# Optimization experiments

Measured on AMD Instinct MI355X. Metric: run time of the kernel, lower is better.

The kernel has to match this reference:

```python
import jax, jax.numpy as jnp
import numpy as np

B, I, H = 32768, 256, 512

def setup_inputs() -> dict:
    key = jax.random.key(0)
    ks = jax.random.split(key, 12)
    s_lstm = 1.0 / np.sqrt(H)
    inp = {
        "inputs": jax.random.normal(ks[0], (B, I), dtype=jnp.float32),
        "h0": jax.random.normal(ks[1], (B, H), dtype=jnp.float32),
        "c0": jax.random.normal(ks[2], (B, H), dtype=jnp.float32),
        "ts": jax.random.uniform(ks[3], (B, 2), dtype=jnp.float32),
        # LSTMCell params (torch layout: [4H, in], gate order i,f,g,o)
        "W_ih": jax.random.uniform(ks[4], (4 * H, I), minval=-s_lstm, maxval=s_lstm, dtype=jnp.float32),
        "W_hh": jax.random.uniform(ks[5], (4 * H, H), minval=-s_lstm, maxval=s_lstm, dtype=jnp.float32),
        "b_ih": jax.random.uniform(ks[6], (4 * H,), minval=-s_lstm, maxval=s_lstm, dtype=jnp.float32),
        "b_hh": jax.random.uniform(ks[7], (4 * H,), minval=-s_lstm, maxval=s_lstm, dtype=jnp.float32),
        # ODE vector field: Linear(H,H) -> Tanh -> Linear(H,H)
        "W1": jax.random.uniform(ks[8], (H, H), minval=-s_lstm, maxval=s_lstm, dtype=jnp.float32),
        "b1": jax.random.uniform(ks[9], (H,), minval=-s_lstm, maxval=s_lstm, dtype=jnp.float32),
        "W2": jax.random.uniform(ks[10], (H, H), minval=-s_lstm, maxval=s_lstm, dtype=jnp.float32),
        "b2": jax.random.uniform(ks[11], (H,), minval=-s_lstm, maxval=s_lstm, dtype=jnp.float32),
    }
    return inp


def _lstm_cell(x, h, c, W_ih, W_hh, b_ih, b_hh):
    z = x @ W_ih.T + b_ih + h @ W_hh.T + b_hh  # [B, 4H]
    i, f, g, o = jnp.split(z, 4, axis=-1)
    i = jax.nn.sigmoid(i)
    f = jax.nn.sigmoid(f)
    g = jnp.tanh(g)
    o = jax.nn.sigmoid(o)
    c2 = f * c + i * g
    h2 = o * jnp.tanh(c2)
    return h2, c2


def reference(inputs, h0, c0, ts, W_ih, W_hh, b_ih, b_hh, W1, b1, W2, b2):
    # two sequential LSTMCell updates with the same input
    h1, c1 = _lstm_cell(inputs, h0, c0, W_ih, W_hh, b_ih, b_hh)
    new_h, new_c = _lstm_cell(inputs, h1, c1, W_ih, W_hh, b_ih, b_hh)

    # autonomous vector field f(h) = W2 tanh(W1 h + b1) + b2
    def f(h):
        return jnp.tanh(h @ W1.T + b1) @ W2.T + b2

    # batched single RK4 step from ts[:,0] to ts[:,1] (fused over batch)
    dt = (ts[:, 1] - ts[:, 0])[:, None]  # [B,1]
    k1 = f(new_h)
    k2 = f(new_h + 0.5 * dt * k1)
    k3 = f(new_h + 0.5 * dt * k2)
    k4 = f(new_h + dt * k3)
    ht = new_h + (dt / 6.0) * (k1 + 2.0 * k2 + 2.0 * k3 + k4)
    return (ht, new_c)
```

## Files before the change

### kernel.cpp

```cpp
#include <hip/hip_runtime.h>
#include <math.h>

#define BATCH 32768
#define ISZ   256
#define HSZ   512
#define KC    768

typedef __attribute__((ext_vector_type(8))) short bf16x8;
typedef __attribute__((ext_vector_type(4))) float f32x4;

static __device__ unsigned short g_xbf[(size_t)BATCH * ISZ];
static __device__ unsigned short g_ha [(size_t)BATCH * HSZ];
static __device__ unsigned short g_hb [(size_t)BATCH * HSZ];
static __device__ float          g_h2f[(size_t)BATCH * HSZ];
static __device__ unsigned short g_Wc [2048 * KC];
static __device__ unsigned short g_W1p[HSZ * HSZ];
static __device__ unsigned short g_W2p[HSZ * HSZ];

__device__ __forceinline__ unsigned short f2bf(float f) {
    unsigned int u = __float_as_uint(f);
    u += 0x7fff + ((u >> 16) & 1);
    return (unsigned short)(u >> 16);
}
__device__ __forceinline__ float bf2f(unsigned short s) {
    return __uint_as_float((unsigned int)s << 16);
}
__device__ __forceinline__ float fsigm(float x) { return 1.0f / (1.0f + __expf(-x)); }
__device__ __forceinline__ float ftanh(float x) { return 1.0f - 2.0f / (__expf(2.0f * x) + 1.0f); }

__device__ __forceinline__ void gload16(const void* g, void* l) {
    __builtin_amdgcn_global_load_lds(
        (const __attribute__((address_space(1))) unsigned int*)g,
        (__attribute__((address_space(3))) unsigned int*)l, 16, 0, 0);
}

template <int DST>
__global__ __launch_bounds__(256) void conv_kernel(
    const float* __restrict__ src, int nv, int w4shift, int dstride, int doff)
{
    unsigned short* __restrict__ dst = DST == 0 ? g_xbf : DST == 1 ? g_ha : g_Wc;
    int i = blockIdx.x * 256 + threadIdx.x;
    const int gs = gridDim.x * 256;
    for (; i < nv; i += gs) {
        const int r = i >> w4shift;
        const int c = i & ((1 << w4shift) - 1);
        const float4 v = ((const float4*)src)[i];
        ushort4 o;
        o.x = f2bf(v.x); o.y = f2bf(v.y); o.z = f2bf(v.z); o.w = f2bf(v.w);
        *(ushort4*)&dst[(size_t)r * dstride + doff + c * 4] = o;
    }
}

template <int DST>
__global__ __launch_bounds__(256) void conv_fragW(const float* __restrict__ src)
{
    unsigned short* __restrict__ dst = DST == 0 ? g_W1p : g_W2p;
    const int c = blockIdx.x * 256 + threadIdx.x;
    const int l15 = c & 15, lq = (c >> 4) & 3, st = (c >> 6) & 15, fb = c >> 10;
    const int n = fb * 16 + l15;
    const int k = st * 32 + lq * 8;
    const float4 v0 = *(const float4*)&src[(size_t)n * HSZ + k];
    const float4 v1 = *(const float4*)&src[(size_t)n * HSZ + k + 4];
    unsigned short o[8] = {f2bf(v0.x), f2bf(v0.y), f2bf(v0.z), f2bf(v0.w),
                           f2bf(v1.x), f2bf(v1.y), f2bf(v1.z), f2bf(v1.w)};
    *(bf16x8*)&dst[(size_t)c * 8] = *(bf16x8*)o;
}

template <int MODE>
__global__ __launch_bounds__(256) void cell_kernel(
    const float* __restrict__ bih, const float* __restrict__ bhh,
    const float* __restrict__ c_in, float* __restrict__ c_out)
{
    constexpr int NKT = KC / 64;
    constexpr int NCH = 16;

    __shared__ __align__(16) unsigned short As[128 * 64];
    __shared__ __align__(16) unsigned short Bs[128 * 64];

    const int orig = blockIdx.x;
    const int q = gridDim.x >> 3;
    const int wg = (orig & 7) * q + (orig >> 3);
    const int nbc = wg % NCH;
    const int mBase = (wg / NCH) * 128;

    const int tid  = threadIdx.x;
    const int lane = tid & 63;
    const int wid  = tid >> 6;
    const int wr   = wid >> 1, wc = wid & 1;
    const int l15  = lane & 15, lq = lane >> 4;

    const unsigned short* __restrict__ Ah = (MODE == 0) ? g_ha : g_hb;

    const int arow = tid >> 3, ch = tid & 7;
    int bgrow[4];
#pragma unroll
    for (int j = 0; j < 4; ++j) {
        const int vr = j * 32 + arow;
        const int g    = (vr >> 4) & 3;
        const int jcol = nbc * 32 + (vr >> 6) * 16 + (vr & 15);
        bgrow[j] = g * 512 + jcol;
    }

    f32x4 acc[4][4];
#pragma unroll
    for (int fm = 0; fm < 4; ++fm)
#pragma unroll
        for (int fn = 0; fn < 4; ++fn) acc[fm][fn] = (f32x4){0.f, 0.f, 0.f, 0.f};

    for (int kt = 0; kt < NKT; ++kt) {
        const int k0 = kt * 64;
#pragma unroll
        for (int j = 0; j < 4; ++j) {
            const int row = j * 32 + arow;
            const unsigned short* ga = (k0 < 256)
                ? g_xbf + (size_t)(mBase + row) * ISZ + (k0       + ch * 8)
                : Ah    + (size_t)(mBase + row) * HSZ + (k0 - 256 + ch * 8);
            gload16(ga, (char*)As + j * 4096 + wid * 1024);
            const unsigned short* gb = g_Wc + (size_t)bgrow[j] * KC + k0 + ch * 8;
            gload16(gb, (char*)Bs + j * 4096 + wid * 1024);
        }
        __syncthreads();
#pragma unroll
        for (int kk = 0; kk < 2; ++kk) {
            bf16x8 a[4], b[4];
#pragma unroll
            for (int f = 0; f < 4; ++f) {
                const int rowA = wr * 64 + f * 16 + l15;
                a[f] = *(const bf16x8*)((const char*)As + rowA * 128 + kk * 64 + lq * 16);
                const int rowB = wc * 64 + f * 16 + l15;
                b[f] = *(const bf16x8*)((const char*)Bs + rowB * 128 + kk * 64 + lq * 16);
            }
#pragma unroll
            for (int fm = 0; fm < 4; ++fm)
#pragma unroll
                for (int fn = 0; fn < 4; ++fn)
                    acc[fm][fn] = __builtin_amdgcn_mfma_f32_16x16x32_bf16(
                        a[fm], b[fn], acc[fm][fn], 0, 0, 0);
        }
        __syncthreads();
    }

    const int j = nbc * 32 + wc * 16 + l15;
    float bsum[4];
#pragma unroll
    for (int g = 0; g < 4; ++g) bsum[g] = bih[g * 512 + j] + bhh[g * 512 + j];
#pragma unroll
    for (int fm = 0; fm < 4; ++fm) {
#pragma unroll
        for (int r = 0; r < 4; ++r) {
            const int m = mBase + wr * 64 + fm * 16 + lq * 4 + r;
            const size_t idx = (size_t)m * HSZ + j;
            const float ig = fsigm(acc[fm][0][r] + bsum[0]);
            const float fg = fsigm(acc[fm][1][r] + bsum[1]);
            const float gg = ftanh(acc[fm][2][r] + bsum[2]);
            const float og = fsigm(acc[fm][3][r] + bsum[3]);
            const float cnew = fg * c_in[idx] + ig * gg;
            const float hnew = og * ftanh(cnew);
            c_out[idx] = cnew;
            if constexpr (MODE == 0) g_hb[idx] = f2bf(hnew);
            else                     g_h2f[idx] = hnew;
        }
    }
}

__global__ __launch_bounds__(512, 1) void rk_fused_kernel(
    const float* __restrict__ ts, const float* __restrict__ b1,
    const float* __restrict__ b2, float* __restrict__ out_ht)
{
    __shared__ __align__(16) unsigned short sU[32 * 512];
    __shared__ __align__(16) unsigned short sH[32 * 512];

    const int tid = threadIdx.x, lane = tid & 63;
    const int w = tid >> 6;
    const int l15 = lane & 15, lq = lane >> 4;
    const int nb = w * 64;
    const int m0 = blockIdx.x * 32;

    float b1v[4], b2v[4];
#pragma unroll
    for (int fn = 0; fn < 4; ++fn) {
        b1v[fn] = b1[nb + fn * 16 + l15];
        b2v[fn] = b2[nb + fn * 16 + l15];
    }

    {
        const float4* __restrict__ src = (const float4*)(g_h2f + (size_t)m0 * HSZ);
#pragma unroll
        for (int i = 0; i < 8; ++i) {
            const int flat = i * 512 + tid;
            const int row = flat >> 7;
            const int c4 = flat & 127;
            const float4 v = src[flat];
            ushort4 o;
            o.x = f2bf(v.x); o.y = f2bf(v.y); o.z = f2bf(v.z); o.w = f2bf(v.w);
            const int off = row * 1024 + ((c4 * 8) ^ ((row & 7) << 4));
            *(ushort4*)((char*)sU + off) = o;
            *(ushort4*)((char*)sH + off) = o;
        }
    }
    __syncthreads();

    f32x4 rk[2][4];
#pragma unroll
    for (int fm = 0; fm < 2; ++fm)
#pragma unroll
        for (int fn = 0; fn < 4; ++fn) rk[fm][fn] = (f32x4){0.f, 0.f, 0.f, 0.f};

    auto loadB = [&](bf16x8 (&bb)[4], const unsigned short* __restrict__ Wp, int st) {
#pragma unroll
        for (int f = 0; f < 4; ++f)
            bb[f] = *(const bf16x8*)(Wp + (size_t)(((w * 4 + f) * 16 + st) * 512 + lane * 8));
    };
    auto loadA = [&](bf16x8 (&aa)[2], int st) {
#pragma unroll
        for (int f = 0; f < 2; ++f) {
            const int row = f * 16 + l15;
            aa[f] = *(const bf16x8*)((const char*)sU + row * 1024 +
                                     ((st * 64 + lq * 16) ^ ((l15 & 7) << 4)));
        }
    };

    auto do_gemm = [&](const unsigned short* __restrict__ Wp, f32x4 (&gacc)[2][4]) {
#pragma unroll
        for (int fm = 0; fm < 2; ++fm)
#pragma unroll
            for (int fn = 0; fn < 4; ++fn) gacc[fm][fn] = (f32x4){0.f, 0.f, 0.f, 0.f};
        bf16x8 b0[4], b1f[4], a[2];
        loadB(b0, Wp, 0);
#pragma unroll 1
        for (int st = 0; st < 16; st += 2) {
            loadB(b1f, Wp, st + 1);
            loadA(a, st);
#pragma unroll
            for (int fm = 0; fm < 2; ++fm)
#pragma unroll
                for (int fn = 0; fn < 4; ++fn)
                    gacc[fm][fn] = __builtin_amdgcn_mfma_f32_16x16x32_bf16(
                        a[fm], b0[fn], gacc[fm][fn], 0, 0, 0);
            __builtin_amdgcn_sched_barrier(0);
            if (st + 2 < 16) loadB(b0, Wp, st + 2);
            loadA(a, st + 1);
#pragma unroll
            for (int fm = 0; fm < 2; ++fm)
#pragma unroll
                for (int fn = 0; fn < 4; ++fn)
                    gacc[fm][fn] = __builtin_amdgcn_mfma_f32_16x16x32_bf16(
                        a[fm], b1f[fn], gacc[fm][fn], 0, 0, 0);
            __builtin_amdgcn_sched_barrier(0);
        }
    };

#pragma unroll 1
    for (int s = 0; s < 4; ++s) {
        f32x4 gacc[2][4];
        do_gemm(g_W1p, gacc);
        __syncthreads();
#pragma unroll
        for (int fm = 0; fm < 2; ++fm)
#pragma unroll
            for (int fn = 0; fn < 4; ++fn)
#pragma unroll
                for (int r = 0; r < 4; ++r) {
                    const int row = fm * 16 + lq * 4 + r;
                    const int col = nb + fn * 16 + l15;
                    *(unsigned short*)((char*)sU + row * 1024 +
                                       ((col * 2) ^ ((row & 7) << 4))) =
                        f2bf(ftanh(gacc[fm][fn][r] + b1v[fn]));
                }
        __syncthreads();
        do_gemm(g_W2p, gacc);
        __syncthreads();
        const float wk = (s == 1 || s == 2) ? 2.0f : 1.0f;
        const float cs = (s == 2) ? 1.0f : 0.5f;
#pragma unroll
        for (int fm = 0; fm < 2; ++fm) {
            float dtf[4];
#pragma unroll
            for (int r = 0; r < 4; ++r) {
                const int m = m0 + fm * 16 + lq * 4 + r;
                const float2 tv = *(const float2*)&ts[2 * m];
                dtf[r] = tv.y - tv.x;
            }
#pragma unroll
            for (int fn = 0; fn < 4; ++fn)
#pragma unroll
                for (int r = 0; r < 4; ++r) {
                    const int row = fm * 16 + lq * 4 + r;
                    const int col = nb + fn * 16 + l15;
                    const float kv = gacc[fm][fn][r] + b2v[fn];
                    rk[fm][fn][r] += wk * kv;
                    if (s < 3) {
                        const int off = row * 1024 + ((col * 2) ^ ((row & 7) << 4));
                        const float h2 = bf2f(*(const unsigned short*)((const char*)sH + off));
                        *(unsigned short*)((char*)sU + off) = f2bf(h2 + cs * dtf[r] * kv);
                    } else {
                        const size_t idx = (size_t)(m0 + row) * HSZ + col;
                        out_ht[idx] = g_h2f[idx] + dtf[r] * (1.0f / 6.0f) * rk[fm][fn][r];
                    }
                }
        }
        if (s < 3) __syncthreads();
    }
}

extern "C" void kernel_launch(void* const* d_in, const int* in_sizes, int n_in,
                              void* d_out, int out_size, void* d_ws, size_t ws_size,
                              hipStream_t stream) {
    const float* x   = (const float*)d_in[0];
    const float* h0  = (const float*)d_in[1];
    const float* c0  = (const float*)d_in[2];
    const float* ts  = (const float*)d_in[3];
    const float* Wih = (const float*)d_in[4];
    const float* Whh = (const float*)d_in[5];
    const float* bih = (const float*)d_in[6];
    const float* bhh = (const float*)d_in[7];
    const float* W1  = (const float*)d_in[8];
    const float* b1  = (const float*)d_in[9];
    const float* W2  = (const float*)d_in[10];
    const float* b2  = (const float*)d_in[11];

    float* out_ht = (float*)d_out;
    float* out_c  = out_ht + (size_t)BATCH * HSZ;

    dim3 blk(256);
    conv_kernel<0><<<2048, blk, 0, stream>>>(x,   BATCH * ISZ / 4, 6, ISZ, 0);
    conv_kernel<1><<<2048, blk, 0, stream>>>(h0,  BATCH * HSZ / 4, 7, HSZ, 0);
    conv_kernel<2><<<256,  blk, 0, stream>>>(Wih, 2048 * 256 / 4,  6, KC, 0);
    conv_kernel<2><<<256,  blk, 0, stream>>>(Whh, 2048 * 512 / 4,  7, KC, 256);
    conv_fragW<0><<<128,  blk, 0, stream>>>(W1);
    conv_fragW<1><<<128,  blk, 0, stream>>>(W2);

    dim3 gcell(BATCH / 128 * 16);

    cell_kernel<0><<<gcell, blk, 0, stream>>>(bih, bhh, c0,    out_c);
    cell_kernel<1><<<gcell, blk, 0, stream>>>(bih, bhh, out_c, out_c);

    rk_fused_kernel<<<BATCH / 32, 512, 0, stream>>>(ts, b1, b2, out_ht);
}
```

Before: 749.4 us.

## Spill RK4 accumulator to output buffer and triple-buffer fully unrolled GEMM B loads

The per-thread RK4 accumulator registers (rk) are removed. The weighted k sum is now accumulated in the global output buffer, and the final value is formed from the bf16 copy of h held in shared memory. This frees 32 VGPRs per thread, which could raise occupancy or give the scheduler more room. In exchange it adds global read-modify-write traffic on every RK stage and uses bf16-rounded h instead of the fp32 h2 for the final add, which may reduce accuracy. The GEMM inner loop is also fully unrolled with a 3-deep rotating B-fragment buffer that prefetches two stages ahead.

```diff
diff --git a/kernel.cpp b/kernel.cpp
--- a/kernel.cpp
+++ b/kernel.cpp
@@ -200,12 +200,6 @@
     }
     __syncthreads();
 
-    f32x4 rk[2][4];
-#pragma unroll
-    for (int fm = 0; fm < 2; ++fm)
-#pragma unroll
-        for (int fn = 0; fn < 4; ++fn) rk[fm][fn] = (f32x4){0.f, 0.f, 0.f, 0.f};
-
     auto loadB = [&](bf16x8 (&bb)[4], const unsigned short* __restrict__ Wp, int st) {
 #pragma unroll
         for (int f = 0; f < 4; ++f)
@@ -225,27 +219,19 @@
         for (int fm = 0; fm < 2; ++fm)
 #pragma unroll
             for (int fn = 0; fn < 4; ++fn) gacc[fm][fn] = (f32x4){0.f, 0.f, 0.f, 0.f};
-        bf16x8 b0[4], b1f[4], a[2];
-        loadB(b0, Wp, 0);
-#pragma unroll 1
-        for (int st = 0; st < 16; st += 2) {
-            loadB(b1f, Wp, st + 1);
+        bf16x8 b[3][4], a[2];
+        loadB(b[0], Wp, 0);
+        loadB(b[1], Wp, 1);
+#pragma unroll
+        for (int st = 0; st < 16; ++st) {
+            if (st + 2 < 16) loadB(b[(st + 2) % 3], Wp, st + 2);
             loadA(a, st);
 #pragma unroll
             for (int fm = 0; fm < 2; ++fm)
 #pragma unroll
                 for (int fn = 0; fn < 4; ++fn)
                     gacc[fm][fn] = __builtin_amdgcn_mfma_f32_16x16x32_bf16(
-                        a[fm], b0[fn], gacc[fm][fn], 0, 0, 0);
-            __builtin_amdgcn_sched_barrier(0);
-            if (st + 2 < 16) loadB(b0, Wp, st + 2);
-            loadA(a, st + 1);
-#pragma unroll
-            for (int fm = 0; fm < 2; ++fm)
-#pragma unroll
-                for (int fn = 0; fn < 4; ++fn)
-                    gacc[fm][fn] = __builtin_amdgcn_mfma_f32_16x16x32_bf16(
-                        a[fm], b1f[fn], gacc[fm][fn], 0, 0, 0);
+                        a[fm], b[st % 3][fn], gacc[fm][fn], 0, 0, 0);
             __builtin_amdgcn_sched_barrier(0);
         }
     };
@@ -270,7 +256,6 @@
         __syncthreads();
         do_gemm(g_W2p, gacc);
         __syncthreads();
-        const float wk = (s == 1 || s == 2) ? 2.0f : 1.0f;
         const float cs = (s == 2) ? 1.0f : 0.5f;
 #pragma unroll
         for (int fm = 0; fm < 2; ++fm) {
@@ -288,14 +273,15 @@
                     const int row = fm * 16 + lq * 4 + r;
                     const int col = nb + fn * 16 + l15;
                     const float kv = gacc[fm][fn][r] + b2v[fn];
-                    rk[fm][fn][r] += wk * kv;
+                    const size_t idx = (size_t)(m0 + row) * HSZ + col;
+                    if (s == 0)      out_ht[idx] = kv;
+                    else if (s < 3)  out_ht[idx] += 2.0f * kv;
+                    const int off = row * 1024 + ((col * 2) ^ ((row & 7) << 4));
+                    const float h2 = bf2f(*(const unsigned short*)((const char*)sH + off));
                     if (s < 3) {
-                        const int off = row * 1024 + ((col * 2) ^ ((row & 7) << 4));
-                        const float h2 = bf2f(*(const unsigned short*)((const char*)sH + off));
                         *(unsigned short*)((char*)sU + off) = f2bf(h2 + cs * dtf[r] * kv);
                     } else {
-                        const size_t idx = (size_t)(m0 + row) * HSZ + col;
-                        out_ht[idx] = g_h2f[idx] + dtf[r] * (1.0f / 6.0f) * rk[fm][fn][r];
+                        out_ht[idx] = h2 + dtf[r] * (1.0f / 6.0f) * (out_ht[idx] + kv);
                     }
                 }
         }
```

After: 1.179 ms. +57.3%, slower.

## Precompute shared input projection x@W_ih once and reuse across both LSTM cells

Applied to the files above, without the earlier changes.

Both LSTM cell updates use the same input x, so the x@W_ih product is split out into a separate kernel. That kernel computes it once and stores it to a global bf16 buffer laid out in fragment order. The two cell kernels now run only the K=512 recurrent GEMM and add the stored projection in the epilogue. This removes one redundant K=256 GEMM pass. In exchange it adds a 128 MB bf16 write and two reads, plus extra bf16 rounding of the input projection before it is summed.

```diff
diff --git a/kernel.cpp b/kernel.cpp
--- a/kernel.cpp
+++ b/kernel.cpp
@@ -13,6 +13,7 @@
 static __device__ unsigned short g_ha [(size_t)BATCH * HSZ];
 static __device__ unsigned short g_hb [(size_t)BATCH * HSZ];
 static __device__ float          g_h2f[(size_t)BATCH * HSZ];
+static __device__ unsigned short g_xw [(size_t)BATCH * 2048];
 static __device__ unsigned short g_Wc [2048 * KC];
 static __device__ unsigned short g_W1p[HSZ * HSZ];
 static __device__ unsigned short g_W2p[HSZ * HSZ];
@@ -66,12 +67,9 @@
     *(bf16x8*)&dst[(size_t)c * 8] = *(bf16x8*)o;
 }
 
-template <int MODE>
-__global__ __launch_bounds__(256) void cell_kernel(
-    const float* __restrict__ bih, const float* __restrict__ bhh,
-    const float* __restrict__ c_in, float* __restrict__ c_out)
+__global__ __launch_bounds__(256) void xw_kernel()
 {
-    constexpr int NKT = KC / 64;
+    constexpr int NKT = 4;
     constexpr int NCH = 16;
 
     __shared__ __align__(16) unsigned short As[128 * 64];
@@ -89,8 +87,6 @@
     const int wr   = wid >> 1, wc = wid & 1;
     const int l15  = lane & 15, lq = lane >> 4;
 
-    const unsigned short* __restrict__ Ah = (MODE == 0) ? g_ha : g_hb;
-
     const int arow = tid >> 3, ch = tid & 7;
     int bgrow[4];
 #pragma unroll
@@ -112,9 +108,7 @@
 #pragma unroll
         for (int j = 0; j < 4; ++j) {
             const int row = j * 32 + arow;
-            const unsigned short* ga = (k0 < 256)
-                ? g_xbf + (size_t)(mBase + row) * ISZ + (k0       + ch * 8)
-                : Ah    + (size_t)(mBase + row) * HSZ + (k0 - 256 + ch * 8);
+            const unsigned short* ga = g_xbf + (size_t)(mBase + row) * ISZ + k0 + ch * 8;
             gload16(ga, (char*)As + j * 4096 + wid * 1024);
             const unsigned short* gb = g_Wc + (size_t)bgrow[j] * KC + k0 + ch * 8;
             gload16(gb, (char*)Bs + j * 4096 + wid * 1024);
@@ -140,6 +134,100 @@
         __syncthreads();
     }
 
+    unsigned short buf[64];
+#pragma unroll
+    for (int fm = 0; fm < 4; ++fm)
+#pragma unroll
+        for (int fn = 0; fn < 4; ++fn)
+#pragma unroll
+            for (int r = 0; r < 4; ++r)
+                buf[(fm * 4 + fn) * 4 + r] = f2bf(acc[fm][fn][r]);
+    unsigned short* dst = g_xw + ((size_t)wg * 256 + tid) * 64;
+#pragma unroll
+    for (int i = 0; i < 8; ++i)
+        ((bf16x8*)dst)[i] = ((const bf16x8*)buf)[i];
+}
+
+template <int MODE>
+__global__ __launch_bounds__(256) void cell_kernel(
+    const float* __restrict__ bih, const float* __restrict__ bhh,
+    const float* __restrict__ c_in, float* __restrict__ c_out)
+{
+    constexpr int NKT = HSZ / 64;
+    constexpr int NCH = 16;
+
+    __shared__ __align__(16) unsigned short As[128 * 64];
+    __shared__ __align__(16) unsigned short Bs[128 * 64];
+
+    const int orig = blockIdx.x;
+    const int q = gridDim.x >> 3;
+    const int wg = (orig & 7) * q + (orig >> 3);
+    const int nbc = wg % NCH;
+    const int mBase = (wg / NCH) * 128;
+
+    const int tid  = threadIdx.x;
+    const int lane = tid & 63;
+    const int wid  = tid >> 6;
+    const int wr   = wid >> 1, wc = wid & 1;
+    const int l15  = lane & 15, lq = lane >> 4;
+
+    const unsigned short* __restrict__ Ah = (MODE == 0) ? g_ha : g_hb;
+
+    const int arow = tid >> 3, ch = tid & 7;
+    int bgrow[4];
+#pragma unroll
+    for (int j = 0; j < 4; ++j) {
+        const int vr = j * 32 + arow;
+        const int g    = (vr >> 4) & 3;
+        const int jcol = nbc * 32 + (vr >> 6) * 16 + (vr & 15);
+        bgrow[j] = g * 512 + jcol;
+    }
+
+    f32x4 acc[4][4];
+#pragma unroll
+    for (int fm = 0; fm < 4; ++fm)
+#pragma unroll
+        for (int fn = 0; fn < 4; ++fn) acc[fm][fn] = (f32x4){0.f, 0.f, 0.f, 0.f};
+
+    for (int kt = 0; kt < NKT; ++kt) {
+        const int k0 = kt * 64;
+#pragma unroll
+        for (int j = 0; j < 4; ++j) {
+            const int row = j * 32 + arow;
+            const unsigned short* ga = Ah + (size_t)(mBase + row) * HSZ + k0 + ch * 8;
+            gload16(ga, (char*)As + j * 4096 + wid * 1024);
+            const unsigned short* gb = g_Wc + (size_t)bgrow[j] * KC + 256 + k0 + ch * 8;
+            gload16(gb, (char*)Bs + j * 4096 + wid * 1024);
+        }
+        __syncthreads();
+#pragma unroll
+        for (int kk = 0; kk < 2; ++kk) {
+            bf16x8 a[4], b[4];
+#pragma unroll
+            for (int f = 0; f < 4; ++f) {
+                const int rowA = wr * 64 + f * 16 + l15;
+                a[f] = *(const bf16x8*)((const char*)As + rowA * 128 + kk * 64 + lq * 16);
+                const int rowB = wc * 64 + f * 16 + l15;
+                b[f] = *(const bf16x8*)((const char*)Bs + rowB * 128 + kk * 64 + lq * 16);
+            }
+#pragma unroll
+            for (int fm = 0; fm < 4; ++fm)
+#pragma unroll
+                for (int fn = 0; fn < 4; ++fn)
+                    acc[fm][fn] = __builtin_amdgcn_mfma_f32_16x16x32_bf16(
+                        a[fm], b[fn], acc[fm][fn], 0, 0, 0);
+        }
+        __syncthreads();
+    }
+
+    unsigned short xwb[64];
+    {
+        const unsigned short* src = g_xw + ((size_t)wg * 256 + tid) * 64;
+#pragma unroll
+        for (int i = 0; i < 8; ++i)
+            ((bf16x8*)xwb)[i] = ((const bf16x8*)src)[i];
+    }
+
     const int j = nbc * 32 + wc * 16 + l15;
     float bsum[4];
 #pragma unroll
@@ -150,10 +238,10 @@
         for (int r = 0; r < 4; ++r) {
             const int m = mBase + wr * 64 + fm * 16 + lq * 4 + r;
             const size_t idx = (size_t)m * HSZ + j;
-            const float ig = fsigm(acc[fm][0][r] + bsum[0]);
-            const float fg = fsigm(acc[fm][1][r] + bsum[1]);
-            const float gg = ftanh(acc[fm][2][r] + bsum[2]);
-            const float og = fsigm(acc[fm][3][r] + bsum[3]);
+            const float ig = fsigm(acc[fm][0][r] + bf2f(xwb[(fm * 4 + 0) * 4 + r]) + bsum[0]);
+            const float fg = fsigm(acc[fm][1][r] + bf2f(xwb[(fm * 4 + 1) * 4 + r]) + bsum[1]);
+            const float gg = ftanh(acc[fm][2][r] + bf2f(xwb[(fm * 4 + 2) * 4 + r]) + bsum[2]);
+            const float og = fsigm(acc[fm][3][r] + bf2f(xwb[(fm * 4 + 3) * 4 + r]) + bsum[3]);
             const float cnew = fg * c_in[idx] + ig * gg;
             const float hnew = og * ftanh(cnew);
             c_out[idx] = cnew;
@@ -332,6 +420,7 @@
 
     dim3 gcell(BATCH / 128 * 16);
 
+    xw_kernel<<<gcell, blk, 0, stream>>>();
     cell_kernel<0><<<gcell, blk, 0, stream>>>(bih, bhh, c0,    out_c);
     cell_kernel<1><<<gcell, blk, 0, stream>>>(bih, bhh, out_c, out_c);
 
```

After: 819.6 us. 1.09x slower.
